# Performance work log

Measured on AMD Instinct MI355X. Metric: run time of the kernel, lower is better.

## Reference

```python
import jax, jax.numpy as jnp
import numpy as np

NUM_LESION_CLS = 8
MAX_INST = 64          # instance ids in mask_gt are < MAX_INST
SIZE_TH = 100.0
# merge_classes=[[1],...,[8]] -> zero-based groups [0..7] => identity merge


def setup_inputs() -> dict:
    key = jax.random.key(0)
    k1, k2, k3 = jax.random.split(key, 3)
    B, H, W, K = 32, 1024, 1024, 64
    pred_class = jax.random.normal(k1, (B, NUM_LESION_CLS), dtype=jnp.float32)
    mask_gt = jax.random.randint(k2, (B, H, W), 0, MAX_INST, dtype=jnp.int32)
    label_gt = jax.random.randint(k3, (B, K, 2), 0, 32, dtype=jnp.int64)
    return {"pred_class": pred_class, "mask_gt": mask_gt, "label_gt": label_gt}


def reference(pred_class, mask_gt, label_gt):
    # Per-sample histogram of instance-id pixel counts: [B, MAX_INST]
    inst_sizes = jax.vmap(lambda m: jnp.bincount(m.reshape(-1), length=MAX_INST))(mask_gt)
    inst_ids = label_gt[..., 0]            # [B, K]
    labels = label_gt[..., 1]              # [B, K]
    sizes = jnp.take_along_axis(inst_sizes, inst_ids, axis=1).astype(jnp.float32)  # [B, K]
    valid = (labels > 0) & (labels <= NUM_LESION_CLS)                              # [B, K]
    # scatter sizes into per-class counts: cnts[b, label-1] += size (if valid)
    onehot = jax.nn.one_hot(jnp.where(valid, labels - 1, 0), NUM_LESION_CLS,
                            dtype=jnp.float32) * valid[..., None].astype(jnp.float32)
    cnts = jnp.einsum('bk,bkc->bc', sizes, onehot)                                 # [B, C]
    # merge_classes is identity here, so class_label == cnts groups
    class_label = jnp.minimum(cnts / SIZE_TH, 1.0)
    # BCEWithLogitsLoss (mean reduction), numerically stable form
    x = pred_class
    loss = jnp.mean(jnp.maximum(x, 0.0) - x * class_label + jnp.log1p(jnp.exp(-jnp.abs(x))))
    return loss
```

## Files before the change

### kernel.cpp

```cpp
#include <hip/hip_runtime.h>
#include <math.h>

#define NB 32
#define HW (1024 * 1024)
#define BINS 64
#define KLBL 64
#define NCLS 8
#define BPI 64
#define TPB 256

__global__ __launch_bounds__(TPB) void hist_kernel(const int* __restrict__ mask,
                                                   int* __restrict__ hist) {
    __shared__ int sh[4][BINS];
    const int tid = threadIdx.x;
    const int b = blockIdx.x / BPI;
    const int part = blockIdx.x % BPI;
    const int wave = tid >> 6;

    sh[tid >> 6][tid & 63] = 0;
    __syncthreads();

    const int4* __restrict__ p = (const int4*)(mask + (size_t)b * HW);
    const int n4 = HW / 4;
    for (int i = part * TPB + tid; i < n4; i += BPI * TPB) {
        int4 v = p[i];
        atomicAdd(&sh[wave][v.x & 63], 1);
        atomicAdd(&sh[wave][v.y & 63], 1);
        atomicAdd(&sh[wave][v.z & 63], 1);
        atomicAdd(&sh[wave][v.w & 63], 1);
    }
    __syncthreads();

    if (tid < BINS) {
        int s = sh[0][tid] + sh[1][tid] + sh[2][tid] + sh[3][tid];
        atomicAdd(&hist[b * BINS + tid], s);
    }
}

__global__ __launch_bounds__(TPB) void finalize_kernel(const float* __restrict__ pred,
                                                       const int* __restrict__ lg,
                                                       const int* __restrict__ hist,
                                                       float* __restrict__ out) {
    __shared__ float cnts[NB * NCLS];
    __shared__ float wsum[4];
    const int tid = threadIdx.x;

    cnts[tid] = 0.0f;
    __syncthreads();

    for (int e = tid; e < NB * KLBL; e += TPB) {
        int inst  = lg[e * 2 + 0];
        int label = lg[e * 2 + 1];
        if (label > 0 && label <= NCLS) {
            float sz = (float)hist[(e >> 6) * BINS + (inst & 63)];
            atomicAdd(&cnts[(e >> 6) * NCLS + (label - 1)], sz);
        }
    }
    __syncthreads();

    float x = pred[tid];
    float t = fminf(cnts[tid] * (1.0f / 100.0f), 1.0f);
    float l = fmaxf(x, 0.0f) - x * t + log1pf(expf(-fabsf(x)));

    for (int off = 32; off > 0; off >>= 1)
        l += __shfl_down(l, off, 64);
    if ((tid & 63) == 0) wsum[tid >> 6] = l;
    __syncthreads();
    if (tid == 0)
        out[0] = (wsum[0] + wsum[1] + wsum[2] + wsum[3]) * (1.0f / (NB * NCLS));
}

extern "C" void kernel_launch(void* const* d_in, const int* in_sizes, int n_in,
                              void* d_out, int out_size, void* d_ws, size_t ws_size,
                              hipStream_t stream) {
    const float* pred = (const float*)d_in[0];
    const int*   mask = (const int*)d_in[1];
    const int*   lg   = (const int*)d_in[2];
    float* out = (float*)d_out;
    int* hist = (int*)d_ws;

    hipMemsetAsync(hist, 0, NB * BINS * sizeof(int), stream);
    hist_kernel<<<NB * BPI, TPB, 0, stream>>>(mask, hist);
    finalize_kernel<<<1, TPB, 0, stream>>>(pred, lg, hist, out);
}
```

Baseline: 210.6 us.

## Use pair histogram to halve LDS atomics in instance-count kernel

Each LDS atomic now counts a pair of pixel values in a 64x64 pair histogram (padded stride 68), so only two atomics are issued per int4 load instead of four. The per-bin counts are rebuilt from row sums and column sums of the pair table, and the loop has a fixed trip count with partial unrolling. The cost is a larger shared-memory footprint (about 17KB per block, which may reduce occupancy), extra zeroing work and an extra reduction phase. Spreading the atomics over 4096 slots also reduces address contention compared with the old four 64-bin copies.

After: 210.1 us. About the same (-0.2%).

```diff
diff --git a/kernel.cpp b/kernel.cpp
--- a/kernel.cpp
+++ b/kernel.cpp
@@ -8,32 +8,53 @@
 #define NCLS 8
 #define BPI 64
 #define TPB 256
+#define PH_STRIDE 68
 
 __global__ __launch_bounds__(TPB) void hist_kernel(const int* __restrict__ mask,
                                                    int* __restrict__ hist) {
-    __shared__ int sh[4][BINS];
+    __shared__ __align__(16) int ph[BINS][PH_STRIDE];
+    __shared__ int rowp[BINS][4];
+    __shared__ int colp[BINS][4];
     const int tid = threadIdx.x;
     const int b = blockIdx.x / BPI;
     const int part = blockIdx.x % BPI;
-    const int wave = tid >> 6;
 
-    sh[tid >> 6][tid & 63] = 0;
+    for (int i = tid; i < BINS * PH_STRIDE; i += TPB) ((int*)ph)[i] = 0;
+    ((int*)rowp)[tid] = 0;
+    ((int*)colp)[tid] = 0;
     __syncthreads();
 
-    const int4* __restrict__ p = (const int4*)(mask + (size_t)b * HW);
-    const int n4 = HW / 4;
-    for (int i = part * TPB + tid; i < n4; i += BPI * TPB) {
-        int4 v = p[i];
-        atomicAdd(&sh[wave][v.x & 63], 1);
-        atomicAdd(&sh[wave][v.y & 63], 1);
-        atomicAdd(&sh[wave][v.z & 63], 1);
-        atomicAdd(&sh[wave][v.w & 63], 1);
+    const int* pm = mask + (size_t)b * HW;
+    const int stride = BPI * TPB;
+    const int base = part * TPB + tid;
+    #pragma unroll 4
+    for (int k = 0; k < 16; ++k) {
+        int4 v = ((const int4*)pm)[base + k * stride];
+        atomicAdd(&((int*)ph)[(v.x & 63) * PH_STRIDE + (v.y & 63)], 1);
+        atomicAdd(&((int*)ph)[(v.z & 63) * PH_STRIDE + (v.w & 63)], 1);
+    }
+    __syncthreads();
+
+    {
+        int a = tid >> 2, q = tid & 3;
+        const int4* r = (const int4*)&ph[a][q * 16];
+        int4 s0 = r[0], s1 = r[1], s2 = r[2], s3 = r[3];
+        rowp[a][q] = s0.x + s0.y + s0.z + s0.w + s1.x + s1.y + s1.z + s1.w
+                   + s2.x + s2.y + s2.z + s2.w + s3.x + s3.y + s3.z + s3.w;
+    }
+    {
+        int bb = tid & 63, pq = tid >> 6;
+        int s = 0;
+        #pragma unroll
+        for (int j = 0; j < 16; ++j) s += ph[pq * 16 + j][bb];
+        colp[bb][pq] = s;
     }
     __syncthreads();
 
     if (tid < BINS) {
-        int s = sh[0][tid] + sh[1][tid] + sh[2][tid] + sh[3][tid];
-        atomicAdd(&hist[b * BINS + tid], s);
+        int t = rowp[tid][0] + rowp[tid][1] + rowp[tid][2] + rowp[tid][3]
+              + colp[tid][0] + colp[tid][1] + colp[tid][2] + colp[tid][3];
+        atomicAdd(&hist[b * BINS + tid], t);
     }
 }
 
```
